# Optimization experiments

Measured on AMD Instinct MI355X. Metric: run time of the kernel, lower is better.

## Reference

```python
import jax, jax.numpy as jnp
import numpy as np

N, K, D = 1_048_576, 16, 8
EPS = 1e-6


def setup_inputs() -> dict:
    key = jax.random.key(0)
    k1, k2, k3, k4 = jax.random.split(key, 4)
    x = jax.random.normal(k1, (N, D), dtype=jnp.float32)
    means = jax.random.normal(k2, (K, D), dtype=jnp.float32)
    # near-identity Cholesky factors so L @ L.T is well conditioned
    chol_var = jnp.broadcast_to(jnp.eye(D, dtype=jnp.float32), (K, D, D)) \
        + 0.05 * jax.random.normal(k3, (K, D, D), dtype=jnp.float32)
    pi = jnp.ones((K,), dtype=jnp.float32) / K \
        + 0.1 * jax.random.uniform(k4, (K,), dtype=jnp.float32)
    return {"x": x, "means": means, "chol_var": chol_var, "pi": pi}


def reference(x, means, chol_var, pi):
    d = x.shape[-1]
    # per-component covariance: tril(L) @ tril(L)^T + eps*I  -> [K, D, D]
    Ltri = jnp.tril(chol_var)
    cov = jnp.einsum('kij,klj->kil', Ltri, Ltri) + EPS * jnp.eye(d, dtype=x.dtype)
    # MultivariateNormal(mean, cov).log_prob == Cholesky of cov + triangular solve
    L = jnp.linalg.cholesky(cov)                                 # [K, D, D]
    diff = x[:, None, :] - means[None, :, :]                     # [N, K, D]
    b = jnp.transpose(diff, (1, 2, 0))                           # [K, D, N]
    y = jax.scipy.linalg.solve_triangular(L, b, lower=True)      # [K, D, N]
    quad = jnp.sum(y * y, axis=1)                                # [K, N]
    half_logdet = jnp.sum(jnp.log(jnp.diagonal(L, axis1=-2, axis2=-1)), axis=-1)  # [K]
    log2pi = jnp.log(jnp.asarray(2.0 * np.pi, dtype=x.dtype))
    log_probs = -0.5 * (quad + d * log2pi) - half_logdet[:, None]  # [K, N]
    # mixture weights via log_softmax, stable logsumexp over components
    weighted = log_probs.T + jax.nn.log_softmax(pi)              # [N, K]
    return jax.nn.logsumexp(weighted, axis=1)                    # [N]
```

## Files before the change

kernel.cpp:

```cpp
#include <hip/hip_runtime.h>
#include <hip/hip_bf16.h>
#include <math.h>

#define KCOMP 16
#define DDIM 8
#define CSTRIDE 48

__global__ void gmm_precompute(const float* __restrict__ means,
                               const float* __restrict__ chol_var,
                               const float* __restrict__ pi,
                               float* __restrict__ coef) {
    int k = threadIdx.x;
    if (k >= KCOMP) return;

    float Lc[DDIM][DDIM];
#pragma unroll
    for (int i = 0; i < DDIM; ++i)
#pragma unroll
        for (int j = 0; j < DDIM; ++j)
            Lc[i][j] = (j <= i) ? chol_var[k * DDIM * DDIM + i * DDIM + j] : 0.0f;

    float C[DDIM][DDIM];
#pragma unroll
    for (int i = 0; i < DDIM; ++i)
#pragma unroll
        for (int j = 0; j < DDIM; ++j) {
            if (j > i) { C[i][j] = 0.0f; continue; }
            float s = 0.0f;
#pragma unroll
            for (int m = 0; m < DDIM; ++m) s += Lc[i][m] * Lc[j][m];
            C[i][j] = s;
        }
#pragma unroll
    for (int i = 0; i < DDIM; ++i) C[i][i] += 1e-6f;

    float L[DDIM][DDIM];
#pragma unroll
    for (int i = 0; i < DDIM; ++i)
#pragma unroll
        for (int j = 0; j < DDIM; ++j) L[i][j] = 0.0f;
#pragma unroll
    for (int j = 0; j < DDIM; ++j) {
        float d = C[j][j];
#pragma unroll
        for (int m = 0; m < DDIM; ++m) if (m < j) d -= L[j][m] * L[j][m];
        float ljj = sqrtf(d);
        L[j][j] = ljj;
        float inv = 1.0f / ljj;
#pragma unroll
        for (int i = 0; i < DDIM; ++i) {
            if (i <= j) continue;
            float s = C[i][j];
#pragma unroll
            for (int m = 0; m < DDIM; ++m) if (m < j) s -= L[i][m] * L[j][m];
            L[i][j] = s * inv;
        }
    }

    float Li[DDIM][DDIM];
#pragma unroll
    for (int i = 0; i < DDIM; ++i)
#pragma unroll
        for (int j = 0; j < DDIM; ++j) Li[i][j] = 0.0f;
#pragma unroll
    for (int c = 0; c < DDIM; ++c) {
        Li[c][c] = 1.0f / L[c][c];
#pragma unroll
        for (int i = 0; i < DDIM; ++i) {
            if (i <= c) continue;
            float s = 0.0f;
#pragma unroll
            for (int m = 0; m < DDIM; ++m)
                if (m >= c && m < i) s += L[i][m] * Li[m][c];
            Li[i][c] = -s / L[i][i];
        }
    }

    float hld = 0.0f;
#pragma unroll
    for (int i = 0; i < DDIM; ++i) hld += logf(L[i][i]);

    float mx = pi[0];
#pragma unroll
    for (int j = 1; j < KCOMP; ++j) mx = fmaxf(mx, pi[j]);
    float ssum = 0.0f;
#pragma unroll
    for (int j = 0; j < KCOMP; ++j) ssum += expf(pi[j] - mx);
    float lse = mx + logf(ssum);

    const float LOG2PI = 1.83787706640934548356f;
    float constk = (pi[k] - lse) - hld - 0.5f * (float)DDIM * LOG2PI;

    const float r = 0.70710678118654752440f;
    float* c = coef + k * CSTRIDE;
    int idx = 0;
#pragma unroll
    for (int i = 0; i < DDIM; ++i)
#pragma unroll
        for (int j = 0; j < DDIM; ++j)
            if (j <= i) c[idx++] = Li[i][j] * r;
#pragma unroll
    for (int i = 0; i < DDIM; ++i) {
        float b = 0.0f;
#pragma unroll
        for (int j = 0; j < DDIM; ++j)
            if (j <= i) b += Li[i][j] * means[k * DDIM + j];
        c[36 + i] = -b * r;
    }
    c[44] = constk;
    c[45] = 0.0f; c[46] = 0.0f; c[47] = 0.0f;
}

__global__ __launch_bounds__(256) void gmm_main(const float* __restrict__ x,
                                                const float* __restrict__ coef,
                                                float* __restrict__ out, int n) {
    int tid = blockIdx.x * 256 + threadIdx.x;
    if (tid >= n) return;

    const float4* xp = (const float4*)(x + (size_t)tid * DDIM);
    float4 a = xp[0];
    float4 b = xp[1];
    float xv[DDIM] = {a.x, a.y, a.z, a.w, b.x, b.y, b.z, b.w};

    float lp[KCOMP];
#pragma unroll
    for (int k = 0; k < KCOMP; ++k) {
        const float* c = coef + k * CSTRIDE;
        float q = 0.0f;
        int idx = 0;
#pragma unroll
        for (int i = 0; i < DDIM; ++i) {
            float y = c[36 + i];
#pragma unroll
            for (int j = 0; j < DDIM; ++j) {
                if (j <= i) { y = fmaf(c[idx], xv[j], y); idx++; }
            }
            q = fmaf(y, y, q);
        }
        lp[k] = c[44] - q;
    }

    float m = lp[0];
#pragma unroll
    for (int k = 1; k < KCOMP; ++k) m = fmaxf(m, lp[k]);
    float s = 0.0f;
#pragma unroll
    for (int k = 0; k < KCOMP; ++k) s += __expf(lp[k] - m);
    out[tid] = m + __logf(s);
}

extern "C" void kernel_launch(void* const* d_in, const int* in_sizes, int n_in,
                              void* d_out, int out_size, void* d_ws, size_t ws_size,
                              hipStream_t stream) {
    const float* x        = (const float*)d_in[0];
    const float* means    = (const float*)d_in[1];
    const float* chol_var = (const float*)d_in[2];
    const float* pi       = (const float*)d_in[3];
    float* out  = (float*)d_out;
    float* coef = (float*)d_ws;

    int n = in_sizes[0] / DDIM;

    gmm_precompute<<<1, 64, 0, stream>>>(means, chol_var, pi, coef);
    gmm_main<<<(n + 255) / 256, 256, 0, stream>>>(x, coef, out, n);
}
```

Measured before the change: 104.3 us.

## Process four points per thread and use a precomputed global max for logsumexp

Each thread now handles four points and walks the sixteen components in a rolled loop, loading each component's coefficients once and reusing them across its points. The per-point max pass of logsumexp is replaced by a single-pass sum that subtracts a max of the per-component constants, computed once in the precompute kernel. This cuts redundant coefficient loads and register pressure from holding all sixteen log-probs. The trade-off is a numerical risk: points far from every mean can underflow the exponentials, and the input loads have no bounds check when n is not a multiple of the tile.

```diff
diff --git a/kernel.cpp b/kernel.cpp
--- a/kernel.cpp
+++ b/kernel.cpp
@@ -5,148 +5,170 @@
 #define KCOMP 16
 #define DDIM 8
 #define CSTRIDE 48
+#define PPT 4
 
 __global__ void gmm_precompute(const float* __restrict__ means,
                                const float* __restrict__ chol_var,
                                const float* __restrict__ pi,
                                float* __restrict__ coef) {
+    __shared__ float sconst[KCOMP];
     int k = threadIdx.x;
-    if (k >= KCOMP) return;
+    if (k < KCOMP) {
+        float Lc[DDIM][DDIM];
+#pragma unroll
+        for (int i = 0; i < DDIM; ++i)
+#pragma unroll
+            for (int j = 0; j < DDIM; ++j)
+                Lc[i][j] = (j <= i) ? chol_var[k * DDIM * DDIM + i * DDIM + j] : 0.0f;
 
-    float Lc[DDIM][DDIM];
+        float C[DDIM][DDIM];
 #pragma unroll
-    for (int i = 0; i < DDIM; ++i)
+        for (int i = 0; i < DDIM; ++i)
 #pragma unroll
-        for (int j = 0; j < DDIM; ++j)
-            Lc[i][j] = (j <= i) ? chol_var[k * DDIM * DDIM + i * DDIM + j] : 0.0f;
+            for (int j = 0; j < DDIM; ++j) {
+                if (j > i) { C[i][j] = 0.0f; continue; }
+                float s = 0.0f;
+#pragma unroll
+                for (int m = 0; m < DDIM; ++m) s += Lc[i][m] * Lc[j][m];
+                C[i][j] = s;
+            }
+#pragma unroll
+        for (int i = 0; i < DDIM; ++i) C[i][i] += 1e-6f;
 
-    float C[DDIM][DDIM];
+        float L[DDIM][DDIM];
 #pragma unroll
-    for (int i = 0; i < DDIM; ++i)
+        for (int i = 0; i < DDIM; ++i)
+#pragma unroll
+            for (int j = 0; j < DDIM; ++j) L[i][j] = 0.0f;
 #pragma unroll
         for (int j = 0; j < DDIM; ++j) {
-            if (j > i) { C[i][j] = 0.0f; continue; }
-            float s = 0.0f;
+            float d = C[j][j];
 #pragma unroll
-            for (int m = 0; m < DDIM; ++m) s += Lc[i][m] * Lc[j][m];
-            C[i][j] = s;
+            for (int m = 0; m < DDIM; ++m) if (m < j) d -= L[j][m] * L[j][m];
+            float ljj = sqrtf(d);
+            L[j][j] = ljj;
+            float inv = 1.0f / ljj;
+#pragma unroll
+            for (int i = 0; i < DDIM; ++i) {
+                if (i <= j) continue;
+                float s = C[i][j];
+#pragma unroll
+                for (int m = 0; m < DDIM; ++m) if (m < j) s -= L[i][m] * L[j][m];
+                L[i][j] = s * inv;
+            }
         }
+
+        float Li[DDIM][DDIM];
 #pragma unroll
-    for (int i = 0; i < DDIM; ++i) C[i][i] += 1e-6f;
+        for (int i = 0; i < DDIM; ++i)
+#pragma unroll
+            for (int j = 0; j < DDIM; ++j) Li[i][j] = 0.0f;
+#pragma unroll
+        for (int c = 0; c < DDIM; ++c) {
+            Li[c][c] = 1.0f / L[c][c];
+#pragma unroll
+            for (int i = 0; i < DDIM; ++i) {
+                if (i <= c) continue;
+                float s = 0.0f;
+#pragma unroll
+                for (int m = 0; m < DDIM; ++m)
+                    if (m >= c && m < i) s += L[i][m] * Li[m][c];
+                Li[i][c] = -s / L[i][i];
+            }
+        }
 
-    float L[DDIM][DDIM];
+        float hld = 0.0f;
 #pragma unroll
-    for (int i = 0; i < DDIM; ++i)
+        for (int i = 0; i < DDIM; ++i) hld += logf(L[i][i]);
+
+        float mx = pi[0];
 #pragma unroll
-        for (int j = 0; j < DDIM; ++j) L[i][j] = 0.0f;
+        for (int j = 1; j < KCOMP; ++j) mx = fmaxf(mx, pi[j]);
+        float ssum = 0.0f;
 #pragma unroll
-    for (int j = 0; j < DDIM; ++j) {
-        float d = C[j][j];
+        for (int j = 0; j < KCOMP; ++j) ssum += expf(pi[j] - mx);
+        float lse = mx + logf(ssum);
+
+        const float LOG2PI = 1.83787706640934548356f;
+        float constk = (pi[k] - lse) - hld - 0.5f * (float)DDIM * LOG2PI;
+
+        const float r = 0.70710678118654752440f;
+        float* c = coef + k * CSTRIDE;
+        int idx = 0;
 #pragma unroll
-        for (int m = 0; m < DDIM; ++m) if (m < j) d -= L[j][m] * L[j][m];
-        float ljj = sqrtf(d);
-        L[j][j] = ljj;
-        float inv = 1.0f / ljj;
+        for (int i = 0; i < DDIM; ++i)
+#pragma unroll
+            for (int j = 0; j < DDIM; ++j)
+                if (j <= i) c[idx++] = Li[i][j] * r;
 #pragma unroll
         for (int i = 0; i < DDIM; ++i) {
-            if (i <= j) continue;
-            float s = C[i][j];
+            float b = 0.0f;
 #pragma unroll
-            for (int m = 0; m < DDIM; ++m) if (m < j) s -= L[i][m] * L[j][m];
-            L[i][j] = s * inv;
+            for (int j = 0; j < DDIM; ++j)
+                if (j <= i) b += Li[i][j] * means[k * DDIM + j];
+            c[36 + i] = -b * r;
         }
+        c[44] = constk;
+        c[45] = 0.0f; c[46] = 0.0f; c[47] = 0.0f;
+        sconst[k] = constk;
     }
-
-    float Li[DDIM][DDIM];
+    __syncthreads();
+    if (threadIdx.x == 0) {
+        float m = sconst[0];
 #pragma unroll
-    for (int i = 0; i < DDIM; ++i)
-#pragma unroll
-        for (int j = 0; j < DDIM; ++j) Li[i][j] = 0.0f;
-#pragma unroll
-    for (int c = 0; c < DDIM; ++c) {
-        Li[c][c] = 1.0f / L[c][c];
-#pragma unroll
-        for (int i = 0; i < DDIM; ++i) {
-            if (i <= c) continue;
-            float s = 0.0f;
-#pragma unroll
-            for (int m = 0; m < DDIM; ++m)
-                if (m >= c && m < i) s += L[i][m] * Li[m][c];
-            Li[i][c] = -s / L[i][i];
-        }
+        for (int j = 1; j < KCOMP; ++j) m = fmaxf(m, sconst[j]);
+        coef[KCOMP * CSTRIDE] = m;
     }
-
-    float hld = 0.0f;
-#pragma unroll
-    for (int i = 0; i < DDIM; ++i) hld += logf(L[i][i]);
-
-    float mx = pi[0];
-#pragma unroll
-    for (int j = 1; j < KCOMP; ++j) mx = fmaxf(mx, pi[j]);
-    float ssum = 0.0f;
-#pragma unroll
-    for (int j = 0; j < KCOMP; ++j) ssum += expf(pi[j] - mx);
-    float lse = mx + logf(ssum);
-
-    const float LOG2PI = 1.83787706640934548356f;
-    float constk = (pi[k] - lse) - hld - 0.5f * (float)DDIM * LOG2PI;
-
-    const float r = 0.70710678118654752440f;
-    float* c = coef + k * CSTRIDE;
-    int idx = 0;
-#pragma unroll
-    for (int i = 0; i < DDIM; ++i)
-#pragma unroll
-        for (int j = 0; j < DDIM; ++j)
-            if (j <= i) c[idx++] = Li[i][j] * r;
-#pragma unroll
-    for (int i = 0; i < DDIM; ++i) {
-        float b = 0.0f;
-#pragma unroll
-        for (int j = 0; j < DDIM; ++j)
-            if (j <= i) b += Li[i][j] * means[k * DDIM + j];
-        c[36 + i] = -b * r;
-    }
-    c[44] = constk;
-    c[45] = 0.0f; c[46] = 0.0f; c[47] = 0.0f;
 }
 
 __global__ __launch_bounds__(256) void gmm_main(const float* __restrict__ x,
                                                 const float* __restrict__ coef,
                                                 float* __restrict__ out, int n) {
-    int tid = blockIdx.x * 256 + threadIdx.x;
-    if (tid >= n) return;
+    const int base = blockIdx.x * (256 * PPT) + threadIdx.x;
 
-    const float4* xp = (const float4*)(x + (size_t)tid * DDIM);
-    float4 a = xp[0];
-    float4 b = xp[1];
-    float xv[DDIM] = {a.x, a.y, a.z, a.w, b.x, b.y, b.z, b.w};
+    float xv[PPT][DDIM];
+#pragma unroll
+    for (int p = 0; p < PPT; ++p) {
+        int pt = base + p * 256;
+        const float4* xp = (const float4*)(x + (size_t)pt * DDIM);
+        float4 a = xp[0];
+        float4 b = xp[1];
+        xv[p][0] = a.x; xv[p][1] = a.y; xv[p][2] = a.z; xv[p][3] = a.w;
+        xv[p][4] = b.x; xv[p][5] = b.y; xv[p][6] = b.z; xv[p][7] = b.w;
+    }
 
-    float lp[KCOMP];
+    const float Cmax = coef[KCOMP * CSTRIDE];
+    float s[PPT];
 #pragma unroll
+    for (int p = 0; p < PPT; ++p) s[p] = 0.0f;
+
+#pragma unroll 1
     for (int k = 0; k < KCOMP; ++k) {
         const float* c = coef + k * CSTRIDE;
-        float q = 0.0f;
-        int idx = 0;
+        float cc[45];
 #pragma unroll
-        for (int i = 0; i < DDIM; ++i) {
-            float y = c[36 + i];
+        for (int t = 0; t < 45; ++t) cc[t] = c[t];
+        const float ck = cc[44] - Cmax;
 #pragma unroll
-            for (int j = 0; j < DDIM; ++j) {
-                if (j <= i) { y = fmaf(c[idx], xv[j], y); idx++; }
+        for (int p = 0; p < PPT; ++p) {
+            float q = 0.0f;
+            int idx = 0;
+#pragma unroll
+            for (int i = 0; i < DDIM; ++i) {
+                float y = cc[36 + i];
+#pragma unroll
+                for (int j = 0; j <= i; ++j) { y = fmaf(cc[idx], xv[p][j], y); ++idx; }
+                q = fmaf(y, y, q);
             }
-            q = fmaf(y, y, q);
+            s[p] += __expf(ck - q);
         }
-        lp[k] = c[44] - q;
     }
 
-    float m = lp[0];
 #pragma unroll
-    for (int k = 1; k < KCOMP; ++k) m = fmaxf(m, lp[k]);
-    float s = 0.0f;
-#pragma unroll
-    for (int k = 0; k < KCOMP; ++k) s += __expf(lp[k] - m);
-    out[tid] = m + __logf(s);
+    for (int p = 0; p < PPT; ++p) {
+        int pt = base + p * 256;
+        if (pt < n) out[pt] = Cmax + __logf(s[p]);
+    }
 }
 
 extern "C" void kernel_launch(void* const* d_in, const int* in_sizes, int n_in,
@@ -162,5 +184,6 @@
     int n = in_sizes[0] / DDIM;
 
     gmm_precompute<<<1, 64, 0, stream>>>(means, chol_var, pi, coef);
-    gmm_main<<<(n + 255) / 256, 256, 0, stream>>>(x, coef, out, n);
+    int nthreads = (n + PPT - 1) / PPT;
+    gmm_main<<<(nthreads + 255) / 256, 256, 0, stream>>>(x, coef, out, n);
 }
```

New measurement: 103.7 us. About the same (-0.6%).
